# Optimization experiments

Measured on AMD Instinct MI355X. Metric: run time of the kernel, lower is better.

Reference implementation:

```python
import jax, jax.numpy as jnp
import numpy as np

D = 1024  # input_size == context_size

def setup_inputs() -> dict:
    key = jax.random.key(0)
    ks = jax.random.split(key, 8)
    B, S = 16, 4096
    s = 1.0 / np.sqrt(D)
    return {
        "x": jax.random.normal(ks[0], (B, S, D), dtype=jnp.float32),
        "context": jax.random.normal(ks[1], (B, D), dtype=jnp.float32),
        "W_in": jax.random.uniform(ks[2], (D, D), jnp.float32, -s, s),
        "b_in": jax.random.uniform(ks[3], (D,), jnp.float32, -s, s),
        "W_ctx": jax.random.uniform(ks[4], (D, D), jnp.float32, -s, s),
        "b_ctx": jax.random.uniform(ks[5], (D,), jnp.float32, -s, s),
        "w_att": jax.random.uniform(ks[6], (D,), jnp.float32, -s, s),
        "b_att": jax.random.uniform(ks[7], (), jnp.float32, -s, s),
    }

def reference(x, context, W_in, b_in, W_ctx, b_ctx, w_att, b_att):
    # projected_input: [B,S,D]; projected_context: [B,D] broadcast over S
    pi = jnp.einsum('bsd,ed->bse', x, W_in) + b_in
    pc = jnp.einsum('bd,ed->be', context, W_ctx) + b_ctx
    h = jnp.tanh(pi + pc[:, None, :])                      # [B,S,D]
    scores = jnp.einsum('bsd,d->bs', h, w_att) + b_att      # [B,S]
    weights = jax.nn.softmax(scores, axis=1)                # [B,S]
    context_vector = jnp.einsum('bs,bsd->bd', weights, x)   # [B,D]
    # dropout is identity in eval mode
    return context_vector
```

## Files before the change

### kernel.cpp

```cpp
#include <hip/hip_runtime.h>
#include <hip/hip_bf16.h>
#include <math.h>

#define NB 16
#define NS 4096
#define ND 1024
#define NM (NB * NS)

#define WS_T       0
#define WS_SCORES  16384
#define WS_WEIGHTS (WS_SCORES + NB * NS)
#define WS_SHARED  (WS_WEIGHTS + NB * NS)
#define WS_XBF16   (WS_SHARED + 524288)
#define WS_SPART   (WS_XBF16 + 33554432)
#define WS_NEED    (((size_t)WS_SPART + 524288) * 4)

typedef short v8s __attribute__((ext_vector_type(8)));
typedef float v4f __attribute__((ext_vector_type(4)));
typedef unsigned short ushort;

#define G_AS __attribute__((address_space(1)))
#define L_AS __attribute__((address_space(3)))

__device__ __forceinline__ ushort f2bf(float f) {
    __hip_bfloat16 h = __float2bfloat16(f);
    return *reinterpret_cast<ushort*>(&h);
}

__device__ __forceinline__ float bf2f(ushort u) {
    return __uint_as_float(((unsigned)u) << 16);
}

__device__ __forceinline__ float fast_tanh(float x) {
    float e = __expf(2.0f * x);
    return 1.0f - 2.0f / (e + 1.0f);
}

__global__ __launch_bounds__(256) void convw_kernel(const float* __restrict__ W,
                                                    ushort* __restrict__ Wb) {
    int flat = blockIdx.x * 256 + threadIdx.x;
#pragma unroll
    for (int j = 0; j < 2; ++j) {
        int idx = flat + j * 131072;
        float4 v = ((const float4*)W)[idx];
        ushort4 o;
        o.x = f2bf(v.x); o.y = f2bf(v.y); o.z = f2bf(v.z); o.w = f2bf(v.w);
        ((ushort4*)Wb)[idx] = o;
    }
}

__global__ __launch_bounds__(256) void convx_kernel(const float* __restrict__ x,
                                                    ushort* __restrict__ xb) {
    size_t base = (size_t)blockIdx.x * 256 + threadIdx.x;
#pragma unroll
    for (int i = 0; i < 16; ++i) {
        size_t idx8 = base + (size_t)i * 524288;
        float4 a = ((const float4*)x)[idx8 * 2];
        float4 c = ((const float4*)x)[idx8 * 2 + 1];
        v8s o;
        o[0] = (short)f2bf(a.x); o[1] = (short)f2bf(a.y);
        o[2] = (short)f2bf(a.z); o[3] = (short)f2bf(a.w);
        o[4] = (short)f2bf(c.x); o[5] = (short)f2bf(c.y);
        o[6] = (short)f2bf(c.z); o[7] = (short)f2bf(c.w);
        ((v8s*)xb)[idx8] = o;
    }
}

__global__ __launch_bounds__(256) void tvec_kernel(const float* __restrict__ context,
                                                   const float* __restrict__ W_ctx,
                                                   const float* __restrict__ b_in,
                                                   const float* __restrict__ b_ctx,
                                                   float* __restrict__ t) {
    __shared__ float ctx[ND];
    int b = blockIdx.y;
    int tid = threadIdx.x;
    for (int i = tid; i < ND; i += 256) ctx[i] = context[b * ND + i];
    __syncthreads();
    int e = blockIdx.x * 64 + (tid >> 2);
    int kq = tid & 3;
    const float4* wr = (const float4*)(W_ctx + (size_t)e * ND + kq * 256);
    const float4* cr = (const float4*)(ctx + kq * 256);
    float acc = 0.f;
#pragma unroll 4
    for (int k = 0; k < 64; ++k) {
        float4 w = wr[k];
        float4 c = cr[k];
        acc += c.x * w.x + c.y * w.y + c.z * w.z + c.w * w.w;
    }
    acc += __shfl_xor(acc, 1);
    acc += __shfl_xor(acc, 2);
    if (kq == 0) t[b * ND + e] = acc + b_in[e] + b_ctx[e];
}

__global__ __launch_bounds__(512) void scores_tile_kernel(const ushort* __restrict__ xbf,
                                                          const ushort* __restrict__ Wb,
                                                          const float* __restrict__ t,
                                                          const float* __restrict__ w_att,
                                                          float* __restrict__ spart) {
    __shared__ ushort As[3][8192];
    __shared__ ushort Bs[3][8192];
    __shared__ float red[8][128];

    int tid = threadIdx.x;
    int o = blockIdx.x;
    int xcd = o & 7, idx = o >> 3;
    int ct = idx & 3;
    int rt = xcd * 32 + (idx >> 2);
    int row0 = rt << 8;
    int e0 = ct << 8;
    int b = row0 >> 12;

    const ushort* gaA0 = xbf + (size_t)(row0 + (tid >> 2)) * ND + (tid & 3) * 8;
    const ushort* gaA1 = gaA0 + (size_t)128 * ND;
    const ushort* gaB0 = Wb + (size_t)(e0 + (tid >> 2)) * ND + (tid & 3) * 8;
    const ushort* gaB1 = gaB0 + (size_t)128 * ND;

    int wid = tid >> 6, l = tid & 63;
    int l15 = l & 15, kq4 = l >> 4;
    int WM = (wid >> 2) * 128;
    int WN = (wid & 3) * 64;

    v4f acc[8][4];
#pragma unroll
    for (int i = 0; i < 8; ++i)
#pragma unroll
        for (int j = 0; j < 4; ++j) acc[i][j] = (v4f)(0.f);

#define STAGE(BUF, KO)                                                                                                 \
    {                                                                                                                  \
        __builtin_amdgcn_global_load_lds((const G_AS void*)(gaA0 + (KO)), (L_AS void*)&As[BUF][tid * 8], 16, 0, 0);    \
        __builtin_amdgcn_global_load_lds((const G_AS void*)(gaA1 + (KO)), (L_AS void*)&As[BUF][(tid + 512) * 8], 16, 0, 0); \
        __builtin_amdgcn_global_load_lds((const G_AS void*)(gaB0 + (KO)), (L_AS void*)&Bs[BUF][tid * 8], 16, 0, 0);    \
        __builtin_amdgcn_global_load_lds((const G_AS void*)(gaB1 + (KO)), (L_AS void*)&Bs[BUF][(tid + 512) * 8], 16, 0, 0); \
    }

#define COMPUTE(BUF)                                                                              \
    {                                                                                             \
        v8s bf[4];                                                                                \
        _Pragma("unroll") for (int nf = 0; nf < 4; ++nf)                                          \
            bf[nf] = *(const v8s*)&Bs[BUF][((WN + nf * 16 + l15) * 4 + kq4) * 8];                 \
        _Pragma("unroll") for (int g = 0; g < 2; ++g) {                                           \
            v8s af[4];                                                                            \
            _Pragma("unroll") for (int j = 0; j < 4; ++j)                                         \
                af[j] = *(const v8s*)&As[BUF][((WM + (g * 4 + j) * 16 + l15) * 4 + kq4) * 8];     \
            _Pragma("unroll") for (int j = 0; j < 4; ++j)                                         \
                _Pragma("unroll") for (int nf = 0; nf < 4; ++nf)                                  \
                    acc[g * 4 + j][nf] = __builtin_amdgcn_mfma_f32_16x16x32_bf16(                 \
                        af[j], bf[nf], acc[g * 4 + j][nf], 0, 0, 0);                              \
        }                                                                                         \
    }

#define KSTEP(KT, BUF, STBUF, VMTOK)                                 \
    {                                                                \
        __builtin_amdgcn_s_barrier();                                \
        STAGE(STBUF, ((KT) + 2) * 32);                               \
        asm volatile("s_waitcnt vmcnt(" VMTOK ")" ::: "memory");     \
        __builtin_amdgcn_s_barrier();                                \
        asm volatile("" ::: "memory");                               \
        COMPUTE(BUF);                                                \
    }

    STAGE(0, 0);
    STAGE(1, 32);

    for (int tt = 0; tt < 10; ++tt) {
        KSTEP(3 * tt + 0, 0, 2, "8");
        KSTEP(3 * tt + 1, 1, 0, "8");
        KSTEP(3 * tt + 2, 2, 1, "8");
    }
    __builtin_amdgcn_s_barrier();
    asm volatile("s_waitcnt vmcnt(4)" ::: "memory");
    __builtin_amdgcn_s_barrier();
    asm volatile("" ::: "memory");
    COMPUTE(0);
    __builtin_amdgcn_s_barrier();
    asm volatile("s_waitcnt vmcnt(0)" ::: "memory");
    __builtin_amdgcn_s_barrier();
    asm volatile("" ::: "memory");
    COMPUTE(1);

#undef KSTEP
#undef COMPUTE
#undef STAGE

    float s[8][4];
#pragma unroll
    for (int i = 0; i < 8; ++i)
#pragma unroll
        for (int j = 0; j < 4; ++j) s[i][j] = 0.f;

#pragma unroll
    for (int nf = 0; nf < 4; ++nf) {
        int e = e0 + WN + nf * 16 + l15;
        float tv = t[b * ND + e];
        float wv = w_att[e];
#pragma unroll
        for (int mf = 0; mf < 8; ++mf)
#pragma unroll
            for (int r = 0; r < 4; ++r)
                s[mf][r] += fast_tanh(acc[mf][nf][r] + tv) * wv;
    }
#pragma unroll
    for (int mf = 0; mf < 8; ++mf)
#pragma unroll
        for (int r = 0; r < 4; ++r) {
            float v = s[mf][r];
            v += __shfl_xor(v, 1);
            v += __shfl_xor(v, 2);
            v += __shfl_xor(v, 4);
            v += __shfl_xor(v, 8);
            s[mf][r] = v;
        }
    if (l15 == 0) {
#pragma unroll
        for (int mf = 0; mf < 8; ++mf)
#pragma unroll
            for (int r = 0; r < 4; ++r)
                red[wid][mf * 16 + kq4 * 4 + r] = s[mf][r];
    }
    __syncthreads();
    if (tid < 256) {
        int mg = tid >> 7;
        int rl = tid & 127;
        float v = red[mg * 4 + 0][rl] + red[mg * 4 + 1][rl] +
                  red[mg * 4 + 2][rl] + red[mg * 4 + 3][rl];
        spart[ct * 65536 + row0 + mg * 128 + rl] = v;
    }
}

__global__ __launch_bounds__(512) void scores_mfma_kernel(const float* __restrict__ x,
                                                          const ushort* __restrict__ Wb,
                                                          const float* __restrict__ t,
                                                          const float* __restrict__ w_att,
                                                          float* __restrict__ scores) {
    __shared__ ushort As[2][64 * 256];
    __shared__ float red[8][64];

    int tid = threadIdx.x;
    int row0 = blockIdx.x * 64;
    int b = row0 >> 12;
    const float4* xf4 = (const float4*)x;

    int sr = tid >> 3;
    int sc = tid & 7;
    int swzbase = (sr & 7) << 3;

    float4 nx[8];
#pragma unroll
    for (int j = 0; j < 8; ++j)
        nx[j] = xf4[(size_t)(row0 + sr) * 256 + sc + j * 8];
#pragma unroll
    for (int j = 0; j < 8; ++j) {
        int c4 = sc + j * 8;
        ushort4 o;
        o.x = f2bf(nx[j].x); o.y = f2bf(nx[j].y); o.z = f2bf(nx[j].z); o.w = f2bf(nx[j].w);
        *(ushort4*)&As[0][sr * 256 + ((c4 * 4) ^ swzbase)] = o;
    }
    __syncthreads();

    int w = tid >> 6;
    int l = tid & 63;
    int l15 = l & 15;
    int kofs = (l >> 4) * 8;
    int xorv = (l & 7) << 3;
    int n0 = w * 128;

    v4f acc[2][4][4];
#pragma unroll
    for (int p = 0; p < 2; ++p)
#pragma unroll
        for (int i = 0; i < 4; ++i)
#pragma unroll
            for (int j = 0; j < 4; ++j) acc[p][i][j] = (v4f)(0.f);

    const ushort* bbase0 = Wb + (size_t)(n0 + l15) * ND + kofs;
    const ushort* bbase1 = bbase0 + (size_t)64 * ND;

#pragma unroll
    for (int kh = 0; kh < 4; ++kh) {
        if (kh < 3) {
#pragma unroll
            for (int j = 0; j < 8; ++j)
                nx[j] = xf4[(size_t)(row0 + sr) * 256 + (kh + 1) * 64 + sc + j * 8];
        }
        const ushort* Ab = &As[kh & 1][0];
        int kb = kh * 256;

        v8s b0c[4], b0n[4], b1[4];
#pragma unroll
        for (int nf = 0; nf < 4; ++nf) b0c[nf] = *(const v8s*)(bbase0 + (size_t)nf * 16 * ND + kb);

#pragma unroll
        for (int ks = 0; ks < 8; ++ks) {
            int kk = kb + ks * 32;
            int elem = (ks * 32 + kofs) ^ xorv;
            v8s af[4];
#pragma unroll
            for (int mf = 0; mf < 4; ++mf)
                af[mf] = *(const v8s*)&Ab[(mf * 16 + l15) * 256 + elem];
#pragma unroll
            for (int nf = 0; nf < 4; ++nf)
                b1[nf] = *(const v8s*)(bbase1 + (size_t)nf * 16 * ND + kk);
            if (ks < 7) {
#pragma unroll
                for (int nf = 0; nf < 4; ++nf)
                    b0n[nf] = *(const v8s*)(bbase0 + (size_t)nf * 16 * ND + kk + 32);
            }
#pragma unroll
            for (int mf = 0; mf < 4; ++mf)
#pragma unroll
                for (int nf = 0; nf < 4; ++nf)
                    acc[0][mf][nf] = __builtin_amdgcn_mfma_f32_16x16x32_bf16(
                        af[mf], b0c[nf], acc[0][mf][nf], 0, 0, 0);
#pragma unroll
            for (int mf = 0; mf < 4; ++mf)
#pragma unroll
                for (int nf = 0; nf < 4; ++nf)
                    acc[1][mf][nf] = __builtin_amdgcn_mfma_f32_16x16x32_bf16(
                        af[mf], b1[nf], acc[1][mf][nf], 0, 0, 0);
#pragma unroll
            for (int nf = 0; nf < 4; ++nf) b0c[nf] = b0n[nf];
        }

        if (kh < 3) {
#pragma unroll
            for (int j = 0; j < 8; ++j) {
                int c4 = sc + j * 8;
                ushort4 o;
                o.x = f2bf(nx[j].x); o.y = f2bf(nx[j].y); o.z = f2bf(nx[j].z); o.w = f2bf(nx[j].w);
                *(ushort4*)&As[(kh + 1) & 1][sr * 256 + ((c4 * 4) ^ swzbase)] = o;
            }
            __syncthreads();
        }
    }

    float s[4][4];
#pragma unroll
    for (int i = 0; i < 4; ++i)
#pragma unroll
        for (int j = 0; j < 4; ++j) s[i][j] = 0.f;

#pragma unroll
    for (int pass = 0; pass < 2; ++pass)
#pragma unroll
        for (int nf = 0; nf < 4; ++nf) {
            int e = n0 + pass * 64 + nf * 16 + l15;
            float tv = t[b * ND + e];
            float wv = w_att[e];
#pragma unroll
            for (int mf = 0; mf < 4; ++mf)
#pragma unroll
                for (int r = 0; r < 4; ++r)
                    s[mf][r] += fast_tanh(acc[pass][mf][nf][r] + tv) * wv;
        }

#pragma unroll
    for (int mf = 0; mf < 4; ++mf)
#pragma unroll
        for (int r = 0; r < 4; ++r) {
            float v = s[mf][r];
            v += __shfl_xor(v, 1);
            v += __shfl_xor(v, 2);
            v += __shfl_xor(v, 4);
            v += __shfl_xor(v, 8);
            s[mf][r] = v;
        }
    if (l15 == 0) {
#pragma unroll
        for (int mf = 0; mf < 4; ++mf)
#pragma unroll
            for (int r = 0; r < 4; ++r)
                red[w][mf * 16 + (l >> 4) * 4 + r] = s[mf][r];
    }
    __syncthreads();
    if (tid < 64) {
        float v = 0.f;
#pragma unroll
        for (int ww = 0; ww < 8; ++ww) v += red[ww][tid];
        scores[(size_t)b * NS + (row0 & (NS - 1)) + tid] = v;
    }
}

__global__ __launch_bounds__(256) void softmax4_kernel(const float* __restrict__ spart,
                                                       float* __restrict__ weights) {
    int b = blockIdx.x;
    int tid = threadIdx.x;
    float v[16];
    float lmax = -1e30f;
#pragma unroll
    for (int i = 0; i < 16; ++i) {
        int grow = b * NS + tid + i * 256;
        float sum = 0.f;
#pragma unroll
        for (int c = 0; c < 4; ++c) sum += spart[c * 65536 + grow];
        v[i] = sum;
        lmax = fmaxf(lmax, sum);
    }
#pragma unroll
    for (int off = 32; off >= 1; off >>= 1) lmax = fmaxf(lmax, __shfl_xor(lmax, off));
    __shared__ float redm[4];
    int wave = tid >> 6;
    if ((tid & 63) == 0) redm[wave] = lmax;
    __syncthreads();
    float bmax = fmaxf(fmaxf(redm[0], redm[1]), fmaxf(redm[2], redm[3]));

    float lsum = 0.f;
#pragma unroll
    for (int i = 0; i < 16; ++i) {
        v[i] = expf(v[i] - bmax);
        lsum += v[i];
    }
#pragma unroll
    for (int off = 32; off >= 1; off >>= 1) lsum += __shfl_xor(lsum, off);
    __shared__ float reds[4];
    if ((tid & 63) == 0) reds[wave] = lsum;
    __syncthreads();
    float inv = 1.0f / (reds[0] + reds[1] + reds[2] + reds[3]);
#pragma unroll
    for (int i = 0; i < 16; ++i) weights[b * NS + tid + i * 256] = v[i] * inv;
}

__global__ __launch_bounds__(256) void softmax_kernel(const float* __restrict__ scores,
                                                      float* __restrict__ weights) {
    int b = blockIdx.x;
    int tid = threadIdx.x;
    float v[16];
    float lmax = -1e30f;
#pragma unroll
    for (int i = 0; i < 16; ++i) {
        v[i] = scores[b * NS + tid + i * 256];
        lmax = fmaxf(lmax, v[i]);
    }
#pragma unroll
    for (int off = 32; off >= 1; off >>= 1) lmax = fmaxf(lmax, __shfl_xor(lmax, off));
    __shared__ float redm[4];
    int wave = tid >> 6;
    if ((tid & 63) == 0) redm[wave] = lmax;
    __syncthreads();
    float bmax = fmaxf(fmaxf(redm[0], redm[1]), fmaxf(redm[2], redm[3]));

    float lsum = 0.f;
#pragma unroll
    for (int i = 0; i < 16; ++i) {
        v[i] = expf(v[i] - bmax);
        lsum += v[i];
    }
#pragma unroll
    for (int off = 32; off >= 1; off >>= 1) lsum += __shfl_xor(lsum, off);
    __shared__ float reds[4];
    if ((tid & 63) == 0) reds[wave] = lsum;
    __syncthreads();
    float inv = 1.0f / (reds[0] + reds[1] + reds[2] + reds[3]);
#pragma unroll
    for (int i = 0; i < 16; ++i) weights[b * NS + tid + i * 256] = v[i] * inv;
}

__global__ __launch_bounds__(256) void wsum_kernel(const float* __restrict__ x,
                                                   const float* __restrict__ w,
                                                   float* __restrict__ part) {
    int sc = blockIdx.x, b = blockIdx.y;
    int d0 = threadIdx.x * 4;
    const float* xb = x + ((size_t)b * NS + sc * 128) * ND;
    const float* wb = w + b * NS + sc * 128;
    float4 acc = {0.f, 0.f, 0.f, 0.f};
    for (int ss = 0; ss < 128; ++ss) {
        float wv = wb[ss];
        float4 xv = *(const float4*)&xb[(size_t)ss * ND + d0];
        acc.x += wv * xv.x;
        acc.y += wv * xv.y;
        acc.z += wv * xv.z;
        acc.w += wv * xv.w;
    }
    *(float4*)&part[(size_t)(b * 32 + sc) * ND + d0] = acc;
}

__global__ __launch_bounds__(256) void wsum_bf_kernel(const ushort* __restrict__ xbf,
                                                      const float* __restrict__ w,
                                                      float* __restrict__ part) {
    int sc = blockIdx.x, b = blockIdx.y;
    int d0 = threadIdx.x * 4;
    const ushort* xb = xbf + ((size_t)b * NS + sc * 128) * ND;
    const float* wb = w + b * NS + sc * 128;
    float4 acc = {0.f, 0.f, 0.f, 0.f};
    for (int ss = 0; ss < 128; ++ss) {
        float wv = wb[ss];
        ushort4 xv = *(const ushort4*)&xb[(size_t)ss * ND + d0];
        acc.x += wv * bf2f(xv.x);
        acc.y += wv * bf2f(xv.y);
        acc.z += wv * bf2f(xv.z);
        acc.w += wv * bf2f(xv.w);
    }
    *(float4*)&part[(size_t)(b * 32 + sc) * ND + d0] = acc;
}

__global__ __launch_bounds__(256) void reduce_kernel(const float* __restrict__ part,
                                                     float* __restrict__ out) {
    int b = blockIdx.x;
    int d0 = threadIdx.x * 4;
    float4 acc = {0.f, 0.f, 0.f, 0.f};
#pragma unroll
    for (int sc = 0; sc < 32; ++sc) {
        float4 v = *(const float4*)&part[(size_t)(b * 32 + sc) * ND + d0];
        acc.x += v.x;
        acc.y += v.y;
        acc.z += v.z;
        acc.w += v.w;
    }
    *(float4*)&out[b * ND + d0] = acc;
}

extern "C" void kernel_launch(void* const* d_in, const int* in_sizes, int n_in,
                              void* d_out, int out_size, void* d_ws, size_t ws_size,
                              hipStream_t stream) {
    const float* x       = (const float*)d_in[0];
    const float* context = (const float*)d_in[1];
    const float* W_in    = (const float*)d_in[2];
    const float* b_in    = (const float*)d_in[3];
    const float* W_ctx   = (const float*)d_in[4];
    const float* b_ctx   = (const float*)d_in[5];
    const float* w_att   = (const float*)d_in[6];

    float* ws      = (float*)d_ws;
    float* t       = ws + WS_T;
    float* scores  = ws + WS_SCORES;
    float* weights = ws + WS_WEIGHTS;
    ushort* wbf16  = (ushort*)(ws + WS_SHARED);
    ushort* xbf16  = (ushort*)(ws + WS_XBF16);
    float* spart   = ws + WS_SPART;
    float* partfb  = ws + WS_SHARED;
    float* out     = (float*)d_out;

    bool fast = ws_size >= WS_NEED;

    convw_kernel<<<dim3(512), 256, 0, stream>>>(W_in, wbf16);
    tvec_kernel<<<dim3(16, NB), 256, 0, stream>>>(context, W_ctx, b_in, b_ctx, t);
    if (fast) {
        convx_kernel<<<dim3(2048), 256, 0, stream>>>(x, xbf16);
        scores_tile_kernel<<<dim3(1024), 512, 0, stream>>>(xbf16, wbf16, t, w_att, spart);
        softmax4_kernel<<<dim3(NB), 256, 0, stream>>>(spart, weights);
        wsum_bf_kernel<<<dim3(32, NB), 256, 0, stream>>>(xbf16, weights, spart);
        reduce_kernel<<<dim3(NB), 256, 0, stream>>>(spart, out);
    } else {
        scores_mfma_kernel<<<dim3(NM / 64), 512, 0, stream>>>(x, wbf16, t, w_att, scores);
        softmax_kernel<<<dim3(NB), 256, 0, stream>>>(scores, weights);
        wsum_kernel<<<dim3(32, NB), 256, 0, stream>>>(x, weights, partfb);
        reduce_kernel<<<dim3(NB), 256, 0, stream>>>(partfb, out);
    }
}
```

Baseline: 282.7 us.

## Restructure GEMM mainloop to double-buffered 64-wide K tiles with XOR swizzle

Result: slower. 310.9 us (+9.9%).

```diff
diff --git a/kernel.cpp b/kernel.cpp
--- a/kernel.cpp
+++ b/kernel.cpp
@@ -97,8 +97,8 @@
                                                           const float* __restrict__ t,
                                                           const float* __restrict__ w_att,
                                                           float* __restrict__ spart) {
-    __shared__ ushort As[3][8192];
-    __shared__ ushort Bs[3][8192];
+    __shared__ ushort As[2][16384];
+    __shared__ ushort Bs[2][16384];
     __shared__ float red[8][128];
 
     int tid = threadIdx.x;
@@ -110,13 +110,13 @@
     int e0 = ct << 8;
     int b = row0 >> 12;
 
-    const ushort* gaA0 = xbf + (size_t)(row0 + (tid >> 2)) * ND + (tid & 3) * 8;
-    const ushort* gaA1 = gaA0 + (size_t)128 * ND;
-    const ushort* gaB0 = Wb + (size_t)(e0 + (tid >> 2)) * ND + (tid & 3) * 8;
-    const ushort* gaB1 = gaB0 + (size_t)128 * ND;
+    int scol = ((tid & 7) ^ ((tid >> 3) & 7)) * 8;
+    const ushort* gA = xbf + (size_t)(row0 + (tid >> 3)) * ND + scol;
+    const ushort* gB = Wb + (size_t)(e0 + (tid >> 3)) * ND + scol;
 
     int wid = tid >> 6, l = tid & 63;
     int l15 = l & 15, kq4 = l >> 4;
+    int l7 = l15 & 7;
     int WM = (wid >> 2) * 128;
     int WN = (wid & 3) * 64;
 
@@ -126,62 +126,66 @@
 #pragma unroll
         for (int j = 0; j < 4; ++j) acc[i][j] = (v4f)(0.f);
 
-#define STAGE(BUF, KO)                                                                                                 \
-    {                                                                                                                  \
-        __builtin_amdgcn_global_load_lds((const G_AS void*)(gaA0 + (KO)), (L_AS void*)&As[BUF][tid * 8], 16, 0, 0);    \
-        __builtin_amdgcn_global_load_lds((const G_AS void*)(gaA1 + (KO)), (L_AS void*)&As[BUF][(tid + 512) * 8], 16, 0, 0); \
-        __builtin_amdgcn_global_load_lds((const G_AS void*)(gaB0 + (KO)), (L_AS void*)&Bs[BUF][tid * 8], 16, 0, 0);    \
-        __builtin_amdgcn_global_load_lds((const G_AS void*)(gaB1 + (KO)), (L_AS void*)&Bs[BUF][(tid + 512) * 8], 16, 0, 0); \
-    }
-
-#define COMPUTE(BUF)                                                                              \
-    {                                                                                             \
-        v8s bf[4];                                                                                \
-        _Pragma("unroll") for (int nf = 0; nf < 4; ++nf)                                          \
-            bf[nf] = *(const v8s*)&Bs[BUF][((WN + nf * 16 + l15) * 4 + kq4) * 8];                 \
-        _Pragma("unroll") for (int g = 0; g < 2; ++g) {                                           \
-            v8s af[4];                                                                            \
-            _Pragma("unroll") for (int j = 0; j < 4; ++j)                                         \
-                af[j] = *(const v8s*)&As[BUF][((WM + (g * 4 + j) * 16 + l15) * 4 + kq4) * 8];     \
-            _Pragma("unroll") for (int j = 0; j < 4; ++j)                                         \
-                _Pragma("unroll") for (int nf = 0; nf < 4; ++nf)                                  \
-                    acc[g * 4 + j][nf] = __builtin_amdgcn_mfma_f32_16x16x32_bf16(                 \
-                        af[j], bf[nf], acc[g * 4 + j][nf], 0, 0, 0);                              \
-        }                                                                                         \
-    }
-
-#define KSTEP(KT, BUF, STBUF, VMTOK)                                 \
-    {                                                                \
-        __builtin_amdgcn_s_barrier();                                \
-        STAGE(STBUF, ((KT) + 2) * 32);                               \
-        asm volatile("s_waitcnt vmcnt(" VMTOK ")" ::: "memory");     \
-        __builtin_amdgcn_s_barrier();                                \
-        asm volatile("" ::: "memory");                               \
-        COMPUTE(BUF);                                                \
-    }
-
-    STAGE(0, 0);
-    STAGE(1, 32);
-
-    for (int tt = 0; tt < 10; ++tt) {
-        KSTEP(3 * tt + 0, 0, 2, "8");
-        KSTEP(3 * tt + 1, 1, 0, "8");
-        KSTEP(3 * tt + 2, 2, 1, "8");
-    }
+#define STAGE_A(SB, H, KO)                                                                              \
+    {                                                                                                   \
+        __builtin_amdgcn_global_load_lds((const G_AS void*)(gA + (size_t)(H) * 128 * ND + (KO)),        \
+                                         (L_AS void*)&As[SB][((H) * 1024 + tid) * 8], 16, 0, 0);        \
+        __builtin_amdgcn_global_load_lds((const G_AS void*)(gA + (size_t)((H) * 128 + 64) * ND + (KO)), \
+                                         (L_AS void*)&As[SB][((H) * 1024 + 512 + tid) * 8], 16, 0, 0);  \
+    }
+#define STAGE_B(SB, H, KO)                                                                              \
+    {                                                                                                   \
+        __builtin_amdgcn_global_load_lds((const G_AS void*)(gB + (size_t)(H) * 128 * ND + (KO)),        \
+                                         (L_AS void*)&Bs[SB][((H) * 1024 + tid) * 8], 16, 0, 0);        \
+        __builtin_amdgcn_global_load_lds((const G_AS void*)(gB + (size_t)((H) * 128 + 64) * ND + (KO)), \
+                                         (L_AS void*)&Bs[SB][((H) * 1024 + 512 + tid) * 8], 16, 0, 0);  \
+    }
+
+#define PHASE(BUF, KK, MH, STMT)                                                                   \
+    {                                                                                              \
+        STMT;                                                                                      \
+        const int kswz = (((KK) * 4 + kq4) ^ l7) * 8;                                              \
+        v8s af[4], bf[4];                                                                          \
+        _Pragma("unroll") for (int j = 0; j < 4; ++j)                                              \
+            af[j] = *(const v8s*)&As[BUF][(WM + ((MH) * 4 + j) * 16 + l15) * 64 + kswz];           \
+        _Pragma("unroll") for (int n = 0; n < 4; ++n)                                              \
+            bf[n] = *(const v8s*)&Bs[BUF][(WN + n * 16 + l15) * 64 + kswz];                        \
+        __builtin_amdgcn_s_barrier();                                                              \
+        __builtin_amdgcn_s_setprio(1);                                                             \
+        _Pragma("unroll") for (int j = 0; j < 4; ++j)                                              \
+            _Pragma("unroll") for (int n = 0; n < 4; ++n)                                          \
+                acc[(MH) * 4 + j][n] = __builtin_amdgcn_mfma_f32_16x16x32_bf16(                    \
+                    af[j], bf[n], acc[(MH) * 4 + j][n], 0, 0, 0);                                  \
+        __builtin_amdgcn_s_setprio(0);                                                             \
+        __builtin_amdgcn_s_barrier();                                                              \
+    }
+
+#define KTILE(BUF, SB, KON, DOST)                                  \
+    PHASE(BUF, 0, 0, if (DOST) STAGE_A(SB, 0, KON));               \
+    PHASE(BUF, 0, 1, if (DOST) STAGE_A(SB, 1, KON));               \
+    PHASE(BUF, 1, 0, if (DOST) STAGE_B(SB, 0, KON));               \
+    PHASE(BUF, 1, 1, if (DOST) STAGE_B(SB, 1, KON));               \
+    asm volatile("s_waitcnt vmcnt(0)" ::: "memory");               \
     __builtin_amdgcn_s_barrier();
-    asm volatile("s_waitcnt vmcnt(4)" ::: "memory");
-    __builtin_amdgcn_s_barrier();
-    asm volatile("" ::: "memory");
-    COMPUTE(0);
-    __builtin_amdgcn_s_barrier();
+
+    STAGE_A(0, 0, 0);
+    STAGE_A(0, 1, 0);
+    STAGE_B(0, 0, 0);
+    STAGE_B(0, 1, 0);
     asm volatile("s_waitcnt vmcnt(0)" ::: "memory");
     __builtin_amdgcn_s_barrier();
-    asm volatile("" ::: "memory");
-    COMPUTE(1);
-
-#undef KSTEP
-#undef COMPUTE
-#undef STAGE
+
+#pragma unroll 1
+    for (int it = 0; it < 8; ++it) {
+        int kbase = it * 128;
+        KTILE(0, 1, kbase + 64, true);
+        KTILE(1, 0, kbase + 128, (it < 7));
+    }
+
+#undef KTILE
+#undef PHASE
+#undef STAGE_B
+#undef STAGE_A
 
     float s[8][4];
 #pragma unroll
```
